# Optimization experiments

Measured on AMD Instinct MI355X. Metric: run time of the kernel, lower is better.

The kernel has to match this reference:

```python
import jax, jax.numpy as jnp
import numpy as np


def setup_inputs() -> dict:
    key = jax.random.key(0)
    k1, k2 = jax.random.split(key)
    B, T, S, D = 8, 1024, 1024, 2048
    support_sets = jax.random.normal(k1, (B, S, D), dtype=jnp.float32)
    X_hats = jax.random.normal(k2, (B, T, D), dtype=jnp.float32)
    return {"support_sets": support_sets, "X_hats": X_hats}


def reference(support_sets, X_hats):
    # Pairwise cosine similarity: out[b, t, s] = cos(X_hats[b, t], support_sets[b, s])
    # Matches torch.nn.functional.cosine_similarity with eps=1e-10:
    #   dot / max(||x|| * ||y||, eps)
    eps = 1e-10
    x_norm = jnp.linalg.norm(X_hats, axis=-1)          # [B, T]
    s_norm = jnp.linalg.norm(support_sets, axis=-1)    # [B, S]
    dots = jnp.einsum('btd,bsd->bts', X_hats, support_sets)  # [B, T, S]
    denom = jnp.maximum(x_norm[:, :, None] * s_norm[:, None, :], eps)
    return dots / denom
```

## Files before the change

### kernel.cpp

```cpp
#include <hip/hip_runtime.h>
#include <hip/hip_bf16.h>

typedef __attribute__((ext_vector_type(4))) float        f32x4;
typedef __attribute__((ext_vector_type(8))) short        s16x8;
typedef __attribute__((ext_vector_type(4))) unsigned int u32x4;
typedef __attribute__((ext_vector_type(2))) unsigned int u32x2;

#define Bb 8
#define Tt 1024
#define Ss 1024
#define Dd 2048
#define BM 128
#define BN 128
#define BK 32

__device__ __forceinline__ unsigned pack2_bf16(float f0, float f1) {
  unsigned u0 = __builtin_bit_cast(unsigned, f0) + 0x8000u;
  unsigned u1 = __builtin_bit_cast(unsigned, f1) + 0x8000u;
  return (u0 >> 16) | (u1 & 0xffff0000u);
}

__device__ __forceinline__ void gld_lds16(const void* g, void* l) {
  __builtin_amdgcn_global_load_lds(
      (__attribute__((address_space(1))) void*)(void*)(g),
      (__attribute__((address_space(3))) void*)l, 16, 0, 0);
}

__global__ __launch_bounds__(256, 4)
void convert_kernel(const float* __restrict__ sup, const float* __restrict__ xh,
                    unsigned* __restrict__ abf, unsigned* __restrict__ bbf,
                    float* __restrict__ invA, float* __restrict__ invB)
{
  const int wave = threadIdx.x >> 6, lane = threadIdx.x & 63;
  const int rowg = blockIdx.x * 4 + wave;
  const float* src; unsigned* dst; float* inv; int row;
  if (rowg < 8192) { row = rowg;         src = xh;  dst = abf; inv = invA; }
  else             { row = rowg - 8192;  src = sup; dst = bbf; inv = invB; }

  const f32x4* s4 = (const f32x4*)(src + (size_t)row * Dd);
  u32x2* d2 = (u32x2*)(dst + (size_t)row * (Dd / 2));
  float sq = 0.0f;
  #pragma unroll
  for (int j = 0; j < 8; ++j) {
    f32x4 v = s4[j * 64 + lane];
    sq = fmaf(v[0], v[0], fmaf(v[1], v[1], fmaf(v[2], v[2], fmaf(v[3], v[3], sq))));
    d2[j * 64 + lane] = (u32x2){pack2_bf16(v[0], v[1]), pack2_bf16(v[2], v[3])};
  }
  #pragma unroll
  for (int m = 32; m; m >>= 1) sq += __shfl_xor(sq, m, 64);
  if (lane == 0) inv[row] = 1.0f / sqrtf(sq);
}

__global__ __launch_bounds__(256, 2)
void gemm_kernel(const short* __restrict__ abf, const short* __restrict__ bbf,
                 const float* __restrict__ invA, const float* __restrict__ invB,
                 float* __restrict__ out)
{
  __shared__ short As[BM * BK];
  __shared__ short Bs[BN * BK];

  const int bid  = blockIdx.x;
  const int b    = bid >> 6;
  const int tile = bid & 63;
  const int tm   = tile >> 3;
  const int tn   = tile & 7;

  const int t = threadIdx.x, wave = t >> 6, lane = t & 63;

  const int srow  = lane >> 2;
  const int cphys = lane & 3;
  const int r0    = wave * 32;
  const int rA0 = r0 + srow, rA1 = r0 + 16 + srow;
  const int cl0 = cphys ^ ((rA0 >> 1) & 3);
  const int cl1 = cphys ^ ((rA1 >> 1) & 3);

  const short* ga0 = abf + (size_t)(b * Tt + tm * BM + rA0) * Dd + cl0 * 8;
  const short* ga1 = abf + (size_t)(b * Tt + tm * BM + rA1) * Dd + cl1 * 8;
  const short* gb0 = bbf + (size_t)(b * Ss + tn * BN + rA0) * Dd + cl0 * 8;
  const short* gb1 = bbf + (size_t)(b * Ss + tn * BN + rA1) * Dd + cl1 * 8;
  short* lA0 = As + r0 * BK;
  short* lA1 = As + (r0 + 16) * BK;
  short* lB0 = Bs + r0 * BK;
  short* lB1 = Bs + (r0 + 16) * BK;

  const int wm = (wave >> 1) << 6;
  const int wn = (wave & 1) << 6;
  const int lm = lane & 15;
  const int kq = lane >> 4;
  const int swk = (kq ^ ((lm >> 1) & 3)) * 8;

  f32x4 acc[4][4];
  #pragma unroll
  for (int i = 0; i < 4; ++i)
    #pragma unroll
    for (int j = 0; j < 4; ++j)
      acc[i][j] = (f32x4)0.0f;

  for (int k0 = 0; k0 < Dd; k0 += BK) {
    __syncthreads();
    gld_lds16(ga0, lA0);
    gld_lds16(ga1, lA1);
    gld_lds16(gb0, lB0);
    gld_lds16(gb1, lB1);
    ga0 += BK; ga1 += BK; gb0 += BK; gb1 += BK;
    __syncthreads();

    s16x8 af[4], bfr[4];
    #pragma unroll
    for (int i = 0; i < 4; ++i) {
      af[i]  = *(const s16x8*)(As + (wm + i * 16 + lm) * BK + swk);
      bfr[i] = *(const s16x8*)(Bs + (wn + i * 16 + lm) * BK + swk);
    }
    #pragma unroll
    for (int mi = 0; mi < 4; ++mi)
      #pragma unroll
      for (int ni = 0; ni < 4; ++ni)
        acc[mi][ni] = __builtin_amdgcn_mfma_f32_16x16x32_bf16(af[mi], bfr[ni], acc[mi][ni], 0, 0, 0);
  }

  const float* iA = invA + b * Tt + tm * BM;
  const float* iB = invB + b * Ss + tn * BN;
  float* outb = out + (size_t)(b * Tt + tm * BM) * Ss + tn * BN;
  const int m0 = wm + kq * 4;
  const int n0 = wn + lm;
  #pragma unroll
  for (int mi = 0; mi < 4; ++mi) {
    #pragma unroll
    for (int r = 0; r < 4; ++r) {
      const int mrow = m0 + mi * 16 + r;
      const float ia = iA[mrow];
      float* orow = outb + (size_t)mrow * Ss;
      #pragma unroll
      for (int ni = 0; ni < 4; ++ni) {
        const int ncol = n0 + ni * 16;
        orow[ncol] = acc[mi][ni][r] * (ia * iB[ncol]);
      }
    }
  }
}

#define LDKF 40
__global__ __launch_bounds__(256, 2)
void paircos_kernel(const float* __restrict__ sup, const float* __restrict__ xh,
                    float* __restrict__ out)
{
  __shared__ short As[BM * LDKF];
  __shared__ short Bs[BN * LDKF];
  __shared__ float invA[BM];
  __shared__ float invB[BN];

  const int bid = blockIdx.x;
  const int b = bid >> 6, tile = bid & 63, tm = tile >> 3, tn = tile & 7;
  const float* Abase = xh  + (size_t)(b * Tt + tm * BM) * Dd;
  const float* Bbase = sup + (size_t)(b * Ss + tn * BN) * Dd;
  const int t = threadIdx.x, row = t >> 1, kh = t & 1;
  const f32x4* agp = (const f32x4*)(Abase + (size_t)row * Dd + kh * 16);
  const f32x4* bgp = (const f32x4*)(Bbase + (size_t)row * Dd + kh * 16);
  u32x4* awr = (u32x4*)(As + row * LDKF + kh * 16);
  u32x4* bwr = (u32x4*)(Bs + row * LDKF + kh * 16);
  const int wave = t >> 6, lane = t & 63;
  const int wm = (wave >> 1) << 6, wn = (wave & 1) << 6;
  const int lm = lane & 15, kq = lane >> 4;

  f32x4 acc[4][4];
  #pragma unroll
  for (int i = 0; i < 4; ++i)
    #pragma unroll
    for (int j = 0; j < 4; ++j) acc[i][j] = (f32x4)0.0f;
  float sqa = 0.0f, sqb = 0.0f;
  f32x4 areg[4], breg[4];
  #pragma unroll
  for (int i = 0; i < 4; ++i) { areg[i] = agp[i]; breg[i] = bgp[i]; }

  for (int k0 = 0; k0 < Dd; k0 += BK) {
    unsigned pa[8], pb[8];
    #pragma unroll
    for (int i = 0; i < 4; ++i) {
      sqa = fmaf(areg[i][0], areg[i][0], sqa); sqa = fmaf(areg[i][1], areg[i][1], sqa);
      sqa = fmaf(areg[i][2], areg[i][2], sqa); sqa = fmaf(areg[i][3], areg[i][3], sqa);
      pa[i*2+0] = pack2_bf16(areg[i][0], areg[i][1]); pa[i*2+1] = pack2_bf16(areg[i][2], areg[i][3]);
      sqb = fmaf(breg[i][0], breg[i][0], sqb); sqb = fmaf(breg[i][1], breg[i][1], sqb);
      sqb = fmaf(breg[i][2], breg[i][2], sqb); sqb = fmaf(breg[i][3], breg[i][3], sqb);
      pb[i*2+0] = pack2_bf16(breg[i][0], breg[i][1]); pb[i*2+1] = pack2_bf16(breg[i][2], breg[i][3]);
    }
    __syncthreads();
    awr[0] = (u32x4){pa[0],pa[1],pa[2],pa[3]}; awr[1] = (u32x4){pa[4],pa[5],pa[6],pa[7]};
    bwr[0] = (u32x4){pb[0],pb[1],pb[2],pb[3]}; bwr[1] = (u32x4){pb[4],pb[5],pb[6],pb[7]};
    __syncthreads();
    if (k0 + BK < Dd) {
      const int off = (k0 + BK) >> 2;
      #pragma unroll
      for (int i = 0; i < 4; ++i) { areg[i] = agp[off + i]; breg[i] = bgp[off + i]; }
    }
    s16x8 af[4], bfr[4];
    #pragma unroll
    for (int i = 0; i < 4; ++i) {
      af[i]  = *(const s16x8*)(As + (wm + i*16 + lm) * LDKF + kq * 8);
      bfr[i] = *(const s16x8*)(Bs + (wn + i*16 + lm) * LDKF + kq * 8);
    }
    #pragma unroll
    for (int mi = 0; mi < 4; ++mi)
      #pragma unroll
      for (int ni = 0; ni < 4; ++ni)
        acc[mi][ni] = __builtin_amdgcn_mfma_f32_16x16x32_bf16(af[mi], bfr[ni], acc[mi][ni], 0, 0, 0);
  }
  __syncthreads();
  ((float*)As)[t] = sqa; ((float*)Bs)[t] = sqb;
  __syncthreads();
  if (t < 128) {
    invA[t] = 1.0f / sqrtf(((float*)As)[2*t] + ((float*)As)[2*t+1]);
    invB[t] = 1.0f / sqrtf(((float*)Bs)[2*t] + ((float*)Bs)[2*t+1]);
  }
  __syncthreads();
  float* outb = out + (size_t)(b * Tt + tm * BM) * Ss + tn * BN;
  const int m0 = wm + kq * 4, n0 = wn + lm;
  #pragma unroll
  for (int mi = 0; mi < 4; ++mi) {
    #pragma unroll
    for (int r = 0; r < 4; ++r) {
      const int mrow = m0 + mi * 16 + r;
      const float ia = invA[mrow];
      float* orow = outb + (size_t)mrow * Ss;
      #pragma unroll
      for (int ni = 0; ni < 4; ++ni) {
        const int ncol = n0 + ni * 16;
        orow[ncol] = acc[mi][ni][r] * (ia * invB[ncol]);
      }
    }
  }
}

extern "C" void kernel_launch(void* const* d_in, const int* in_sizes, int n_in,
                              void* d_out, int out_size, void* d_ws, size_t ws_size,
                              hipStream_t stream) {
  const float* sup = (const float*)d_in[0];
  const float* xh  = (const float*)d_in[1];
  float* out = (float*)d_out;

  const size_t nElem = (size_t)Bb * Tt * Dd;
  const size_t bfBytes = nElem * sizeof(short);
  const size_t NEED = 2 * bfBytes + 2 * (size_t)Bb * Tt * sizeof(float);

  if (ws_size >= NEED) {
    unsigned* abf = (unsigned*)d_ws;
    unsigned* bbf = (unsigned*)((char*)d_ws + bfBytes);
    float* invA = (float*)((char*)d_ws + 2 * bfBytes);
    float* invB = invA + (size_t)Bb * Tt;
    convert_kernel<<<dim3(4096), dim3(256), 0, stream>>>(sup, xh, abf, bbf, invA, invB);
    gemm_kernel<<<dim3(512), dim3(256), 0, stream>>>((const short*)abf, (const short*)bbf,
                                                     invA, invB, out);
  } else {
    paircos_kernel<<<dim3(512), dim3(256), 0, stream>>>(sup, xh, out);
  }
}
```

Measured before the change: 210.0 us.

## Double GEMM K-tile to 64 with 8-way XOR swizzle; two rows per convert wave

```diff
diff --git a/kernel.cpp b/kernel.cpp
--- a/kernel.cpp
+++ b/kernel.cpp
@@ -12,7 +12,7 @@
 #define Dd 2048
 #define BM 128
 #define BN 128
-#define BK 32
+#define BK 64
 
 __device__ __forceinline__ unsigned pack2_bf16(float f0, float f1) {
   unsigned u0 = __builtin_bit_cast(unsigned, f0) + 0x8000u;
@@ -32,23 +32,28 @@
                     float* __restrict__ invA, float* __restrict__ invB)
 {
   const int wave = threadIdx.x >> 6, lane = threadIdx.x & 63;
-  const int rowg = blockIdx.x * 4 + wave;
+  const int rowg = (blockIdx.x * 4 + wave) * 2;
   const float* src; unsigned* dst; float* inv; int row;
   if (rowg < 8192) { row = rowg;         src = xh;  dst = abf; inv = invA; }
   else             { row = rowg - 8192;  src = sup; dst = bbf; inv = invB; }
 
-  const f32x4* s4 = (const f32x4*)(src + (size_t)row * Dd);
-  u32x2* d2 = (u32x2*)(dst + (size_t)row * (Dd / 2));
-  float sq = 0.0f;
+  const f32x4* s0 = (const f32x4*)(src + (size_t)row * Dd);
+  const f32x4* s1 = (const f32x4*)(src + (size_t)(row + 1) * Dd);
+  u32x2* d0 = (u32x2*)(dst + (size_t)row * (Dd / 2));
+  u32x2* d1 = (u32x2*)(dst + (size_t)(row + 1) * (Dd / 2));
+  float sq0 = 0.0f, sq1 = 0.0f;
   #pragma unroll
   for (int j = 0; j < 8; ++j) {
-    f32x4 v = s4[j * 64 + lane];
-    sq = fmaf(v[0], v[0], fmaf(v[1], v[1], fmaf(v[2], v[2], fmaf(v[3], v[3], sq))));
-    d2[j * 64 + lane] = (u32x2){pack2_bf16(v[0], v[1]), pack2_bf16(v[2], v[3])};
-  }
-  #pragma unroll
-  for (int m = 32; m; m >>= 1) sq += __shfl_xor(sq, m, 64);
-  if (lane == 0) inv[row] = 1.0f / sqrtf(sq);
+    f32x4 v0 = s0[j * 64 + lane];
+    f32x4 v1 = s1[j * 64 + lane];
+    sq0 = fmaf(v0[0], v0[0], fmaf(v0[1], v0[1], fmaf(v0[2], v0[2], fmaf(v0[3], v0[3], sq0))));
+    sq1 = fmaf(v1[0], v1[0], fmaf(v1[1], v1[1], fmaf(v1[2], v1[2], fmaf(v1[3], v1[3], sq1))));
+    d0[j * 64 + lane] = (u32x2){pack2_bf16(v0[0], v0[1]), pack2_bf16(v0[2], v0[3])};
+    d1[j * 64 + lane] = (u32x2){pack2_bf16(v1[0], v1[1]), pack2_bf16(v1[2], v1[3])};
+  }
+  #pragma unroll
+  for (int m = 32; m; m >>= 1) { sq0 += __shfl_xor(sq0, m, 64); sq1 += __shfl_xor(sq1, m, 64); }
+  if (lane == 0) { inv[row] = 1.0f / sqrtf(sq0); inv[row + 1] = 1.0f / sqrtf(sq1); }
 }
 
 __global__ __launch_bounds__(256, 2)
@@ -67,27 +72,37 @@
 
   const int t = threadIdx.x, wave = t >> 6, lane = t & 63;
 
-  const int srow  = lane >> 2;
-  const int cphys = lane & 3;
-  const int r0    = wave * 32;
-  const int rA0 = r0 + srow, rA1 = r0 + 16 + srow;
-  const int cl0 = cphys ^ ((rA0 >> 1) & 3);
-  const int cl1 = cphys ^ ((rA1 >> 1) & 3);
-
-  const short* ga0 = abf + (size_t)(b * Tt + tm * BM + rA0) * Dd + cl0 * 8;
-  const short* ga1 = abf + (size_t)(b * Tt + tm * BM + rA1) * Dd + cl1 * 8;
-  const short* gb0 = bbf + (size_t)(b * Ss + tn * BN + rA0) * Dd + cl0 * 8;
-  const short* gb1 = bbf + (size_t)(b * Ss + tn * BN + rA1) * Dd + cl1 * 8;
-  short* lA0 = As + r0 * BK;
-  short* lA1 = As + (r0 + 16) * BK;
-  short* lB0 = Bs + r0 * BK;
-  short* lB1 = Bs + (r0 + 16) * BK;
+  const int srow = lane >> 3;
+  const int cph  = lane & 7;
+  const int r0   = wave * 32;
+
+  const size_t aRow = (size_t)(b * Tt + tm * BM);
+  const size_t bRow = (size_t)(b * Ss + tn * BN);
+  const short *gA0, *gA1, *gA2, *gA3, *gB0, *gB1, *gB2, *gB3;
+  {
+    int r;
+    r = r0 + 0 * 8 + srow; gA0 = abf + (aRow + r) * Dd + (cph ^ (r & 7)) * 8;
+                           gB0 = bbf + (bRow + r) * Dd + (cph ^ (r & 7)) * 8;
+    r = r0 + 1 * 8 + srow; gA1 = abf + (aRow + r) * Dd + (cph ^ (r & 7)) * 8;
+                           gB1 = bbf + (bRow + r) * Dd + (cph ^ (r & 7)) * 8;
+    r = r0 + 2 * 8 + srow; gA2 = abf + (aRow + r) * Dd + (cph ^ (r & 7)) * 8;
+                           gB2 = bbf + (bRow + r) * Dd + (cph ^ (r & 7)) * 8;
+    r = r0 + 3 * 8 + srow; gA3 = abf + (aRow + r) * Dd + (cph ^ (r & 7)) * 8;
+                           gB3 = bbf + (bRow + r) * Dd + (cph ^ (r & 7)) * 8;
+  }
+  short* lA0 = As + (r0 + 0)  * BK;
+  short* lA1 = As + (r0 + 8)  * BK;
+  short* lA2 = As + (r0 + 16) * BK;
+  short* lA3 = As + (r0 + 24) * BK;
+  short* lB0 = Bs + (r0 + 0)  * BK;
+  short* lB1 = Bs + (r0 + 8)  * BK;
+  short* lB2 = Bs + (r0 + 16) * BK;
+  short* lB3 = Bs + (r0 + 24) * BK;
 
   const int wm = (wave >> 1) << 6;
   const int wn = (wave & 1) << 6;
   const int lm = lane & 15;
   const int kq = lane >> 4;
-  const int swk = (kq ^ ((lm >> 1) & 3)) * 8;
 
   f32x4 acc[4][4];
   #pragma unroll
@@ -98,24 +113,27 @@
 
   for (int k0 = 0; k0 < Dd; k0 += BK) {
     __syncthreads();
-    gld_lds16(ga0, lA0);
-    gld_lds16(ga1, lA1);
-    gld_lds16(gb0, lB0);
-    gld_lds16(gb1, lB1);
-    ga0 += BK; ga1 += BK; gb0 += BK; gb1 += BK;
-    __syncthreads();
-
-    s16x8 af[4], bfr[4];
-    #pragma unroll
-    for (int i = 0; i < 4; ++i) {
-      af[i]  = *(const s16x8*)(As + (wm + i * 16 + lm) * BK + swk);
-      bfr[i] = *(const s16x8*)(Bs + (wn + i * 16 + lm) * BK + swk);
-    }
-    #pragma unroll
-    for (int mi = 0; mi < 4; ++mi)
-      #pragma unroll
-      for (int ni = 0; ni < 4; ++ni)
-        acc[mi][ni] = __builtin_amdgcn_mfma_f32_16x16x32_bf16(af[mi], bfr[ni], acc[mi][ni], 0, 0, 0);
+    gld_lds16(gA0, lA0); gld_lds16(gA1, lA1); gld_lds16(gA2, lA2); gld_lds16(gA3, lA3);
+    gld_lds16(gB0, lB0); gld_lds16(gB1, lB1); gld_lds16(gB2, lB2); gld_lds16(gB3, lB3);
+    gA0 += BK; gA1 += BK; gA2 += BK; gA3 += BK;
+    gB0 += BK; gB1 += BK; gB2 += BK; gB3 += BK;
+    __syncthreads();
+
+    #pragma unroll
+    for (int ks = 0; ks < 2; ++ks) {
+      const int pchunk = ((ks * 4 + kq) ^ (lm & 7)) * 8;
+      s16x8 af[4], bfr[4];
+      #pragma unroll
+      for (int i = 0; i < 4; ++i) {
+        af[i]  = *(const s16x8*)(As + (wm + i * 16 + lm) * BK + pchunk);
+        bfr[i] = *(const s16x8*)(Bs + (wn + i * 16 + lm) * BK + pchunk);
+      }
+      #pragma unroll
+      for (int mi = 0; mi < 4; ++mi)
+        #pragma unroll
+        for (int ni = 0; ni < 4; ++ni)
+          acc[mi][ni] = __builtin_amdgcn_mfma_f32_16x16x32_bf16(af[mi], bfr[ni], acc[mi][ni], 0, 0, 0);
+    }
   }
 
   const float* iA = invA + b * Tt + tm * BM;
@@ -140,6 +158,7 @@
 }
 
 #define LDKF 40
+#define BKF 32
 __global__ __launch_bounds__(256, 2)
 void paircos_kernel(const float* __restrict__ sup, const float* __restrict__ xh,
                     float* __restrict__ out)
@@ -172,7 +191,7 @@
   #pragma unroll
   for (int i = 0; i < 4; ++i) { areg[i] = agp[i]; breg[i] = bgp[i]; }
 
-  for (int k0 = 0; k0 < Dd; k0 += BK) {
+  for (int k0 = 0; k0 < Dd; k0 += BKF) {
     unsigned pa[8], pb[8];
     #pragma unroll
     for (int i = 0; i < 4; ++i) {
@@ -187,8 +206,8 @@
     awr[0] = (u32x4){pa[0],pa[1],pa[2],pa[3]}; awr[1] = (u32x4){pa[4],pa[5],pa[6],pa[7]};
     bwr[0] = (u32x4){pb[0],pb[1],pb[2],pb[3]}; bwr[1] = (u32x4){pb[4],pb[5],pb[6],pb[7]};
     __syncthreads();
-    if (k0 + BK < Dd) {
-      const int off = (k0 + BK) >> 2;
+    if (k0 + BKF < Dd) {
+      const int off = (k0 + BKF) >> 2;
       #pragma unroll
       for (int i = 0; i < 4; ++i) { areg[i] = agp[off + i]; breg[i] = bgp[off + i]; }
     }
@@ -246,7 +265,7 @@
     unsigned* bbf = (unsigned*)((char*)d_ws + bfBytes);
     float* invA = (float*)((char*)d_ws + 2 * bfBytes);
     float* invB = invA + (size_t)Bb * Tt;
-    convert_kernel<<<dim3(4096), dim3(256), 0, stream>>>(sup, xh, abf, bbf, invA, invB);
+    convert_kernel<<<dim3(2048), dim3(256), 0, stream>>>(sup, xh, abf, bbf, invA, invB);
     gemm_kernel<<<dim3(512), dim3(256), 0, stream>>>((const short*)abf, (const short*)bbf,
                                                      invA, invB, out);
   } else {
```

Measured after the change: 202.9 us. 3.4% less time.
